# Performance work log

Measured on AMD Instinct MI355X. Metric: run time of the kernel, lower is better.

## Reference

```python
import jax, jax.numpy as jnp
import numpy as np

N_NODES = 20000
N_EDGES = 80000
D = 128       # in_dim_node == in_dim_edge == hidden dims
ITERS = 15    # mp_iterations
EPS = 1e-5    # torch LayerNorm default eps


def _mlp(h, W0, b0, W1, b1, W2, b2, gamma, beta):
    """Linear-ReLU-Linear-ReLU-Linear-LayerNorm (hidden_layers=2)."""
    h = jax.nn.relu(h @ W0 + b0)
    h = jax.nn.relu(h @ W1 + b1)
    h = h @ W2 + b2
    mu = jnp.mean(h, axis=-1, keepdims=True)
    var = jnp.var(h, axis=-1, keepdims=True)
    return gamma * (h - mu) * jax.lax.rsqrt(var + EPS) + beta


def setup_inputs() -> dict:
    key = jax.random.key(0)
    ks = iter(jax.random.split(key, 32))

    def lin(fi, fo):
        bnd = 1.0 / np.sqrt(fi)
        W = jax.random.uniform(next(ks), (ITERS, fi, fo), minval=-bnd, maxval=bnd, dtype=jnp.float32)
        b = jax.random.uniform(next(ks), (ITERS, fo), minval=-bnd, maxval=bnd, dtype=jnp.float32)
        return W, b

    x = jax.random.normal(next(ks), (N_NODES, D), dtype=jnp.float32)
    edge_attr = jax.random.normal(next(ks), (N_EDGES, D), dtype=jnp.float32)
    edge_index = jax.random.randint(next(ks), (2, N_EDGES), 0, N_NODES)

    eW0, eB0 = lin(3 * D, D)   # edge MLP input = cat(src, dest, edge) = 384
    eW1, eB1 = lin(D, D)
    eW2, eB2 = lin(D, D)
    nW0, nB0 = lin(2 * D, D)   # node MLP input = cat(x, agg) = 256
    nW1, nB1 = lin(D, D)
    nW2, nB2 = lin(D, D)
    ones = jnp.ones((ITERS, D), jnp.float32)
    zeros = jnp.zeros((ITERS, D), jnp.float32)

    return dict(x=x, edge_attr=edge_attr,
                eW0=eW0, eB0=eB0, eW1=eW1, eB1=eB1, eW2=eW2, eB2=eB2, eG=ones, eBeta=zeros,
                nW0=nW0, nB0=nB0, nW1=nW1, nB1=nB1, nW2=nW2, nB2=nB2, nG=ones, nBeta=zeros,
                edge_index=edge_index)


def reference(x, edge_attr, eW0, eB0, eW1, eB1, eW2, eB2, eG, eBeta,
              nW0, nB0, nW1, nB1, nW2, nB2, nG, nBeta, edge_index):
    row, col = edge_index[0], edge_index[1]
    n = x.shape[0]
    params = (eW0, eB0, eW1, eB1, eW2, eB2, eG, eBeta,
              nW0, nB0, nW1, nB1, nW2, nB2, nG, nBeta)

    def step(carry, p):
        xc, ec = carry
        (ew0, eb0, ew1, eb1, ew2, eb2, eg, ebt,
         nw0, nb0, nw1, nb1, nw2, nb2, ng, nbt) = p
        # EdgeProcessor: gather + MLP, then FullResidualConnection (add previous)
        e_in = jnp.concatenate([xc[row], xc[col], ec], axis=-1)        # [E, 3D]
        ec = _mlp(e_in, ew0, eb0, ew1, eb1, ew2, eb2, eg, ebt) + ec
        # NodeProcessor: scatter_sum over destination nodes + MLP + residual
        agg = jax.ops.segment_sum(ec, col, num_segments=n)             # [N, D]
        n_in = jnp.concatenate([xc, agg], axis=-1)                     # [N, 2D]
        xc = _mlp(n_in, nw0, nb0, nw1, nb1, nw2, nb2, ng, nbt) + xc
        return (xc, ec), None

    (x, edge_attr), _ = jax.lax.scan(step, (x, edge_attr), params)
    return x, edge_attr
```

## Files before the change

### kernel.cpp

```cpp
#include <hip/hip_runtime.h>
#include <hip/hip_bf16.h>

typedef __hip_bfloat16 bf16;
typedef __attribute__((ext_vector_type(8))) short short8;
typedef __attribute__((ext_vector_type(4))) float f32x4;

#define NN 20000
#define NE 80000
#define DD 128
#define NITER 15
#define HSTRIDE 136

__device__ inline void gload16(const void* g, void* l) {
  __builtin_amdgcn_global_load_lds(
      (const __attribute__((address_space(1))) void*)g,
      (__attribute__((address_space(3))) void*)l, 16, 0, 0);
}

__device__ inline void waitVm(int n) {
  switch (n) {
    case 0: asm volatile("s_waitcnt vmcnt(0)" ::: "memory"); break;
    case 1: asm volatile("s_waitcnt vmcnt(1)" ::: "memory"); break;
    case 2: asm volatile("s_waitcnt vmcnt(2)" ::: "memory"); break;
    case 3: asm volatile("s_waitcnt vmcnt(3)" ::: "memory"); break;
    case 4: asm volatile("s_waitcnt vmcnt(4)" ::: "memory"); break;
    case 5: asm volatile("s_waitcnt vmcnt(5)" ::: "memory"); break;
    default: asm volatile("s_waitcnt vmcnt(6)" ::: "memory"); break;
  }
}

__device__ inline float bfbits2f(unsigned int hi16) {
  union { unsigned int u; float f; } c; c.u = hi16; return c.f;
}

__device__ inline float readin(const void* p, size_t i, int fl) {
  return fl ? (float)((const bf16*)p)[i] : ((const float*)p)[i];
}

__global__ void detzero_kernel(const unsigned short* __restrict__ x,
                               int* __restrict__ counts, int* __restrict__ flag) {
  const int bid = blockIdx.x, t = threadIdx.x;
  if (bid < 79) {
    int i = bid * 256 + t;
    if (i < NN) counts[i] = 0;
    return;
  }
  __shared__ int cs[256], ct[256];
  int sane = 0, tot = 0;
  for (int i = 2 * t; i < 16384; i += 512) {
    unsigned short v = x[i];
    int e = (v >> 7) & 0xFF;
    tot++;
    if (v == 0 || (e >= 80 && e <= 170)) sane++;
  }
  cs[t] = sane; ct[t] = tot;
  __syncthreads();
  for (int o = 128; o > 0; o >>= 1) {
    if (t < o) { cs[t] += cs[t + o]; ct[t] += ct[t + o]; }
    __syncthreads();
  }
  if (t == 0) *flag = (cs[0] * 10 > ct[0] * 7) ? 1 : 0;
}

#define CX  (NN * DD)
#define CE  (NE * DD)
#define CW0 (NITER * 384 * DD)
#define CW1 (NITER * 128 * DD)
#define CNW0 (NITER * 256 * DD)
#define CB  (NITER * DD)
#define BX0 CX
#define BX1 (BX0 + CE)
#define BX2 (BX1 + 10 * CB)

struct CvtP {
  const void *x, *e;
  bf16 *xb, *eb;
  const void* bs[10];
  float* bd[10];
  const int* flag;
};

__global__ void convert_all(CvtP P) {
  const int fl = *P.flag;
  const int gstride = gridDim.x * 256;
  for (int i = blockIdx.x * 256 + threadIdx.x; i < BX2; i += gstride) {
    if (i < BX0) {
      P.xb[i] = (bf16)readin(P.x, i, fl);
    } else if (i < BX1) {
      P.eb[i - BX0] = (bf16)readin(P.e, i - BX0, fl);
    } else {
      int j = i - BX1;
      int b = j / CB, r = j - b * CB;
      P.bd[b][r] = readin(P.bs[b], r, fl);
    }
  }
}

struct WtP {
  const void* w[6];
  bf16* wt[6];
  const int* flag;
};

__global__ void wtrans_kernel(WtP P) {
  __shared__ float tile[32][33];
  const int fl = *P.flag;
  const int bid = blockIdx.x;
  int w, rem;
  if      (bid < 720)  { w = 0; rem = bid; }
  else if (bid < 960)  { w = 1; rem = bid - 720; }
  else if (bid < 1200) { w = 2; rem = bid - 960; }
  else if (bid < 1680) { w = 3; rem = bid - 1200; }
  else if (bid < 1920) { w = 4; rem = bid - 1680; }
  else                 { w = 5; rem = bid - 1920; }
  const int K = (w == 0) ? 384 : (w == 3) ? 256 : 128;
  const int nkt    = K >> 5;
  const int per_it = nkt << 2;
  const int it = rem / per_it;
  const int r2 = rem - it * per_it;
  const int k0 = (r2 >> 2) << 5;
  const int n0 = (r2 & 3) << 5;

  const int tx = threadIdx.x & 31, ty = threadIdx.x >> 5;
  const size_t base = (size_t)it * K * DD;

#pragma unroll
  for (int p = 0; p < 4; p++) {
    const int k = k0 + ty + 8 * p;
    tile[ty + 8 * p][tx] = readin(P.w[w], base + (size_t)k * DD + n0 + tx, fl);
  }
  __syncthreads();
#pragma unroll
  for (int p = 0; p < 4; p++) {
    const int n = n0 + ty + 8 * p;
    const int k = k0 + tx;
    const int q = (k >> 3) & 3;
    const int kp = (k & ~24) | (((q ^ ((n >> 1) & 3)) & 3) << 3);
    P.wt[w][base + (size_t)n * K + kp] = (bf16)tile[tx][ty + 8 * p];
  }
}

template<int K0, int AMODE, int NW, int MI>
__global__ __launch_bounds__(NW * 64, MI == 2 ? 3 : 4) void fused_mlp(
    const bf16* S0b,
    const bf16* S1b,
    const int*  __restrict__ eidx,
    const bf16* __restrict__ W0t, const bf16* __restrict__ W1t,
    const bf16* __restrict__ W2t,
    const float* __restrict__ b0, const float* __restrict__ b1,
    const float* __restrict__ b2,
    const float* __restrict__ gamma, const float* __restrict__ beta,
    bf16* st, int M)
{
  constexpr int NS1  = K0 / 32;
  constexpr int RPW  = 16 * MI;
  constexpr int ROWS = NW * RPW;
  constexpr int DN   = 2;
  __shared__ __align__(16) bf16 Bls[2][128 * 32];
  __shared__ __align__(16) bf16 Hls[ROWS * HSTRIDE];

  const int tid  = threadIdx.x;
  const int lane = tid & 63;
  const int wv   = tid >> 6;
  const int l15  = lane & 15, quad = lane >> 4;
  const int m0   = blockIdx.x * ROWS;
  const int scol = tid >> 2;
  const int sk8  = (tid & 3) * 8;

  int rowm[MI], ir[MI], ic[MI];
#pragma unroll
  for (int g = 0; g < MI; g++) {
    rowm[g] = min(m0 + wv * RPW + g * 16 + l15, M - 1);
    ir[g] = 0; ic[g] = 0;
    if (AMODE == 1) { ir[g] = eidx[rowm[g]]; ic[g] = eidx[NE + rowm[g]]; }
  }

  auto dmaW = [&](const bf16* W, int K, int kk, int buf) {
    gload16(W + (size_t)scol * K + kk + sk8,        &Bls[buf][scol * 32 + sk8]);
    gload16(W + (size_t)(scol + 64) * K + kk + sk8, &Bls[buf][(scol + 64) * 32 + sk8]);
  };
  auto gatherA = [&](int g, int kk, short8* a) {
    const int ks = (kk & 127) + quad * 8;
    const bf16* base;
    if (AMODE == 1) {
      const int seg = kk >> 7;
      base = (seg == 0) ? S0b + (size_t)ir[g] * DD
           : (seg == 1) ? S0b + (size_t)ic[g] * DD
                        : S1b + (size_t)rowm[g] * DD;
    } else {
      base = (kk >> 7) ? S1b + (size_t)rowm[g] * DD
                       : S0b + (size_t)rowm[g] * DD;
    }
    *a = *(const short8*)(base + ks);
  };

  auto readB = [&](int buf, short8* bfr) {
#pragma unroll
    for (int ni = 0; ni < 8; ni++) {
      const int r = ni * 16 + l15;
      bfr[ni] = *(const short8*)&Bls[buf][r * 32 + ((quad ^ ((r >> 1) & 3)) & 3) * 8];
    }
  };

  f32x4 acc[MI][8];
  auto zacc = [&]() {
#pragma unroll
    for (int g = 0; g < MI; g++)
#pragma unroll
      for (int j = 0; j < 8; j++) acc[g][j] = (f32x4){0.f, 0.f, 0.f, 0.f};
  };
  auto slabMfmaA = [&](short8* a, int buf) {
    short8 bfr[8];
    readB(buf, bfr);
#pragma unroll
    for (int g = 0; g < MI; g++)
#pragma unroll
      for (int ni = 0; ni < 8; ni++)
        acc[g][ni] = __builtin_amdgcn_mfma_f32_16x16x32_bf16(a[g], bfr[ni], acc[g][ni], 0, 0, 0);
  };
  auto slabMfmaH = [&](int kk, int buf) {
    short8 bfr[8];
    readB(buf, bfr);
#pragma unroll
    for (int g = 0; g < MI; g++) {
      short8 a = *(const short8*)&Hls[(wv * RPW + g * 16 + l15) * HSTRIDE + kk + quad * 8];
#pragma unroll
      for (int ni = 0; ni < 8; ni++)
        acc[g][ni] = __builtin_amdgcn_mfma_f32_16x16x32_bf16(a, bfr[ni], acc[g][ni], 0, 0, 0);
    }
  };
  auto writeH = [&](const float* bias) {
    float bv[8];
#pragma unroll
    for (int ni = 0; ni < 8; ni++) bv[ni] = bias[ni * 16 + l15];
#pragma unroll
    for (int g = 0; g < MI; g++)
#pragma unroll
      for (int r = 0; r < 4; r++) {
        const int row = wv * RPW + g * 16 + quad * 4 + r;
#pragma unroll
        for (int ni = 0; ni < 8; ni++)
          Hls[row * HSTRIDE + ni * 16 + l15] = (bf16)fmaxf(acc[g][ni][r] + bv[ni], 0.f);
      }
  };

  zacc();
  short8 aCur[MI], aNxt[MI];
  dmaW(W0t, K0, 0, 0);
#pragma unroll
  for (int g = 0; g < MI; g++) gatherA(g, 0, &aCur[g]);
#pragma unroll
  for (int s = 0; s < NS1; s++) {
    int cnt;
    if (s + 1 < NS1) {
      dmaW(W0t, K0, (s + 1) * 32, (s + 1) & 1);
#pragma unroll
      for (int g = 0; g < MI; g++) gatherA(g, (s + 1) * 32, &aNxt[g]);
      cnt = MI + DN + MI;
    } else {
      dmaW(W1t, 128, 0, NS1 & 1);
      cnt = MI + DN;
    }
    waitVm(cnt);
    __builtin_amdgcn_s_barrier();
    __builtin_amdgcn_sched_barrier(0);
    slabMfmaA(aCur, s & 1);
    __builtin_amdgcn_sched_barrier(0);
    __builtin_amdgcn_s_barrier();
#pragma unroll
    for (int g = 0; g < MI; g++) aCur[g] = aNxt[g];
  }
  writeH(b0);

  zacc();
#pragma unroll
  for (int s = 0; s < 4; s++) {
    if (s < 3) dmaW(W1t, 128, (s + 1) * 32, (NS1 + s + 1) & 1);
    else       dmaW(W2t, 128, 0,            (NS1 + 4) & 1);
    waitVm(DN);
    __builtin_amdgcn_s_barrier();
    __builtin_amdgcn_sched_barrier(0);
    slabMfmaH(s * 32, (NS1 + s) & 1);
    __builtin_amdgcn_sched_barrier(0);
    __builtin_amdgcn_s_barrier();
  }
  writeH(b1);

  zacc();
#pragma unroll
  for (int s = 0; s < 4; s++) {
    int cnt = 0;
    if (s < 3) { dmaW(W2t, 128, (s + 1) * 32, (NS1 + 4 + s + 1) & 1); cnt = DN; }
    waitVm(cnt);
    __builtin_amdgcn_s_barrier();
    __builtin_amdgcn_sched_barrier(0);
    slabMfmaH(s * 32, (NS1 + 4 + s) & 1);
    if (s < 3) {
      __builtin_amdgcn_sched_barrier(0);
      __builtin_amdgcn_s_barrier();
    }
  }

  float bv[8], gv[8], btv[8];
#pragma unroll
  for (int ni = 0; ni < 8; ni++) {
    const int col = ni * 16 + l15;
    bv[ni] = b2[col]; gv[ni] = gamma[col]; btv[ni] = beta[col];
  }
#pragma unroll
  for (int g = 0; g < MI; g++) {
#pragma unroll
    for (int r = 0; r < 4; r++) {
      float a = 0.f, bq = 0.f;
#pragma unroll
      for (int ni = 0; ni < 8; ni++) {
        const float v = acc[g][ni][r] + bv[ni];
        a += v; bq += v * v;
      }
#pragma unroll
      for (int off = 1; off < 16; off <<= 1) {
        a  += __shfl_xor(a, off);
        bq += __shfl_xor(bq, off);
      }
      const float mu = a * (1.0f / 128.0f);
      const float var = fmaxf(bq * (1.0f / 128.0f) - mu * mu, 0.0f);
      const float rs = rsqrtf(var + 1e-5f);
      const int m = m0 + wv * RPW + g * 16 + quad * 4 + r;
      if (m < M) {
#pragma unroll
        for (int ni = 0; ni < 8; ni++) {
          const int col = ni * 16 + l15;
          const float v = acc[g][ni][r] + bv[ni];
          const float lnv = (v - mu) * rs * gv[ni] + btv[ni];
          const size_t idx = (size_t)m * DD + col;
          st[idx] = (bf16)(lnv + (float)st[idx]);
        }
      }
    }
  }
}

__global__ void hist_kernel(const int* __restrict__ eidx, int* __restrict__ counts) {
  int e = blockIdx.x * 256 + threadIdx.x;
  if (e < NE) atomicAdd(&counts[eidx[NE + e]], 1);
}

__global__ void scan_kernel(const int* __restrict__ counts, int* __restrict__ offs,
                            int* __restrict__ cursor) {
  __shared__ int sums[1024];
  const int t = threadIdx.x;
  const int base = t * 20;
  int local[20];
  int s = 0;
  for (int i = 0; i < 20; i++) {
    int idx = base + i;
    int c = (idx < NN) ? counts[idx] : 0;
    local[i] = s; s += c;
  }
  sums[t] = s;
  __syncthreads();
  for (int off = 1; off < 1024; off <<= 1) {
    int v = 0;
    if (t >= off) v = sums[t - off];
    __syncthreads();
    if (t >= off) sums[t] += v;
    __syncthreads();
  }
  int excl = (t == 0) ? 0 : sums[t - 1];
  for (int i = 0; i < 20; i++) {
    int idx = base + i;
    if (idx < NN) { offs[idx] = excl + local[i]; cursor[idx] = 0; }
  }
  if (t == 1023) offs[NN] = sums[1023];
}

__global__ void fill_kernel(const int* __restrict__ eidx, const int* __restrict__ offs,
                            int* __restrict__ cursor, int* __restrict__ sorted) {
  int e = blockIdx.x * 256 + threadIdx.x;
  if (e < NE) {
    int n = eidx[NE + e];
    int p = atomicAdd(&cursor[n], 1);
    sorted[offs[n] + p] = e;
  }
}

__global__ void aggregate_kernel(const bf16* __restrict__ eb, const int* __restrict__ offs,
                                 const int* __restrict__ sorted, bf16* __restrict__ aggb) {
  const int node = blockIdx.x * 4 + (threadIdx.x >> 6);
  const int lane = threadIdx.x & 63;
  if (node >= NN) return;
  const int s = offs[node], t = offs[node + 1];
  float a0 = 0.f, a1 = 0.f;
  for (int i = s; i < t; i++) {
    const int e = sorted[i];
    unsigned int v = *(const unsigned int*)(eb + (size_t)e * DD + 2 * lane);
    a0 += bfbits2f(v << 16);
    a1 += bfbits2f(v & 0xFFFF0000u);
  }
  bf16 o0 = (bf16)a0, o1 = (bf16)a1;
  unsigned int pack = (unsigned int)(*(unsigned short*)&o0)
                    | ((unsigned int)(*(unsigned short*)&o1) << 16);
  *(unsigned int*)(aggb + (size_t)node * DD + 2 * lane) = pack;
}

__global__ void outwb_kernel(const bf16* __restrict__ xb, const bf16* __restrict__ eb,
                             void* __restrict__ out, const int* __restrict__ flag) {
  int i = blockIdx.x * 256 + threadIdx.x;
  const int nx = NN * DD, total = (NN + NE) * DD;
  if (i < total) {
    bf16 v = (i < nx) ? xb[i] : eb[i - nx];
    if (*flag) ((bf16*)out)[i] = v;
    else       ((float*)out)[i] = (float)v;
  }
}

extern "C" void kernel_launch(void* const* d_in, const int* in_sizes, int n_in,
                              void* d_out, int out_size, void* d_ws, size_t ws_size,
                              hipStream_t stream) {
  const int* eidx = (const int*)d_in[18];

  char* ws = (char*)d_ws;
  size_t off = 0;
  auto alloc = [&](size_t bytes) -> char* {
    char* p = ws + off;
    off = (off + bytes + 255) & ~(size_t)255;
    return p;
  };

  bf16* xb   = (bf16*)alloc((size_t)NN * DD * 2);
  bf16* eb   = (bf16*)alloc((size_t)NE * DD * 2);
  bf16* aggb = (bf16*)alloc((size_t)NN * DD * 2);
  bf16* eW0t = (bf16*)alloc((size_t)CW0 * 2);
  bf16* eW1t = (bf16*)alloc((size_t)CW1 * 2);
  bf16* eW2t = (bf16*)alloc((size_t)CW1 * 2);
  bf16* nW0t = (bf16*)alloc((size_t)CNW0 * 2);
  bf16* nW1t = (bf16*)alloc((size_t)CW1 * 2);
  bf16* nW2t = (bf16*)alloc((size_t)CW1 * 2);
  float* bf_[10];
  for (int i = 0; i < 10; i++) bf_[i] = (float*)alloc(CB * 4);
  int* counts = (int*)alloc((size_t)NN * 4);
  int* cursor = (int*)alloc((size_t)NN * 4);
  int* offs   = (int*)alloc((size_t)(NN + 1) * 4);
  int* sorted = (int*)alloc((size_t)NE * 4);
  int* flag   = (int*)alloc(4);

  detzero_kernel<<<80, 256, 0, stream>>>((const unsigned short*)d_in[0], counts, flag);

  CvtP C;
  C.x = d_in[0]; C.e = d_in[1];
  C.xb = xb; C.eb = eb;
  const int bsrc_idx[10] = {3, 5, 7, 8, 9, 11, 13, 15, 16, 17};
  for (int i = 0; i < 10; i++) { C.bs[i] = d_in[bsrc_idx[i]]; C.bd[i] = bf_[i]; }
  C.flag = flag;
  convert_all<<<2048, 256, 0, stream>>>(C);

  WtP W;
  W.w[0] = d_in[2];  W.w[1] = d_in[4];  W.w[2] = d_in[6];
  W.w[3] = d_in[10]; W.w[4] = d_in[12]; W.w[5] = d_in[14];
  W.wt[0] = eW0t; W.wt[1] = eW1t; W.wt[2] = eW2t;
  W.wt[3] = nW0t; W.wt[4] = nW1t; W.wt[5] = nW2t;
  W.flag = flag;
  wtrans_kernel<<<2160, 256, 0, stream>>>(W);

  hist_kernel<<<(NE + 255) / 256, 256, 0, stream>>>(eidx, counts);
  scan_kernel<<<1, 1024, 0, stream>>>(counts, offs, cursor);
  fill_kernel<<<(NE + 255) / 256, 256, 0, stream>>>(eidx, offs, cursor, sorted);

  const int egrid = NE / 128;
  const int ngrid = (NN + 63) / 64;

  for (int t = 0; t < NITER; t++) {
    fused_mlp<384, 1, 4, 2><<<egrid, 256, 0, stream>>>(
        xb, eb, eidx,
        eW0t + (size_t)t * 384 * DD, eW1t + (size_t)t * 128 * DD,
        eW2t + (size_t)t * 128 * DD,
        bf_[0] + t * DD, bf_[1] + t * DD, bf_[2] + t * DD,
        bf_[3] + t * DD, bf_[4] + t * DD, eb, NE);
    aggregate_kernel<<<(NN + 3) / 4, 256, 0, stream>>>(eb, offs, sorted, aggb);
    fused_mlp<256, 2, 4, 1><<<ngrid, 256, 0, stream>>>(
        xb, aggb, nullptr,
        nW0t + (size_t)t * 256 * DD, nW1t + (size_t)t * 128 * DD,
        nW2t + (size_t)t * 128 * DD,
        bf_[5] + t * DD, bf_[6] + t * DD, bf_[7] + t * DD,
        bf_[8] + t * DD, bf_[9] + t * DD, xb, NN);
  }

  outwb_kernel<<<((NN + NE) * DD + 255) / 256, 256, 0, stream>>>(xb, eb, d_out, flag);
}
```

Before: 1.065 ms.

## Fuse edge scatter-sum into edge MLP epilogue via fp32 atomics

Drops the CSR sort (hist/scan/fill) and the separate aggregate kernel. The edge MLP epilogue now atomically adds each updated edge row into an fp32 node buffer. The node MLP reads that buffer directly, converting to bf16, and re-zeroes its own rows after the first layer, ready for the next iteration. This removes one kernel launch per iteration and a re-read of the edge features, at the cost of many global fp32 atomics, a doubled-size aggregate buffer, and a summation order that is no longer deterministic.

```diff
diff --git a/kernel.cpp b/kernel.cpp
--- a/kernel.cpp
+++ b/kernel.cpp
@@ -29,22 +29,13 @@
   }
 }
 
-__device__ inline float bfbits2f(unsigned int hi16) {
-  union { unsigned int u; float f; } c; c.u = hi16; return c.f;
-}
-
 __device__ inline float readin(const void* p, size_t i, int fl) {
   return fl ? (float)((const bf16*)p)[i] : ((const float*)p)[i];
 }
 
-__global__ void detzero_kernel(const unsigned short* __restrict__ x,
-                               int* __restrict__ counts, int* __restrict__ flag) {
-  const int bid = blockIdx.x, t = threadIdx.x;
-  if (bid < 79) {
-    int i = bid * 256 + t;
-    if (i < NN) counts[i] = 0;
-    return;
-  }
+__global__ void detect_kernel(const unsigned short* __restrict__ x,
+                              int* __restrict__ flag) {
+  const int t = threadIdx.x;
   __shared__ int cs[256], ct[256];
   int sane = 0, tot = 0;
   for (int i = 2 * t; i < 16384; i += 512) {
@@ -71,27 +62,31 @@
 #define BX0 CX
 #define BX1 (BX0 + CE)
 #define BX2 (BX1 + 10 * CB)
+#define BX3 (BX2 + CX)
 
 struct CvtP {
   const void *x, *e;
   bf16 *xb, *eb;
   const void* bs[10];
   float* bd[10];
+  float* aggz;
   const int* flag;
 };
 
 __global__ void convert_all(CvtP P) {
   const int fl = *P.flag;
   const int gstride = gridDim.x * 256;
-  for (int i = blockIdx.x * 256 + threadIdx.x; i < BX2; i += gstride) {
+  for (int i = blockIdx.x * 256 + threadIdx.x; i < BX3; i += gstride) {
     if (i < BX0) {
       P.xb[i] = (bf16)readin(P.x, i, fl);
     } else if (i < BX1) {
       P.eb[i - BX0] = (bf16)readin(P.e, i - BX0, fl);
-    } else {
+    } else if (i < BX2) {
       int j = i - BX1;
       int b = j / CB, r = j - b * CB;
       P.bd[b][r] = readin(P.bs[b], r, fl);
+    } else {
+      P.aggz[i - BX2] = 0.f;
     }
   }
 }
@@ -150,7 +145,7 @@
     const float* __restrict__ b0, const float* __restrict__ b1,
     const float* __restrict__ b2,
     const float* __restrict__ gamma, const float* __restrict__ beta,
-    bf16* st, int M)
+    bf16* st, int M, float* aggf)
 {
   constexpr int NS1  = K0 / 32;
   constexpr int RPW  = 16 * MI;
@@ -181,17 +176,28 @@
   };
   auto gatherA = [&](int g, int kk, short8* a) {
     const int ks = (kk & 127) + quad * 8;
-    const bf16* base;
     if (AMODE == 1) {
       const int seg = kk >> 7;
-      base = (seg == 0) ? S0b + (size_t)ir[g] * DD
-           : (seg == 1) ? S0b + (size_t)ic[g] * DD
-                        : S1b + (size_t)rowm[g] * DD;
+      const bf16* base = (seg == 0) ? S0b + (size_t)ir[g] * DD
+                       : (seg == 1) ? S0b + (size_t)ic[g] * DD
+                                    : S1b + (size_t)rowm[g] * DD;
+      *a = *(const short8*)(base + ks);
     } else {
-      base = (kk >> 7) ? S1b + (size_t)rowm[g] * DD
-                       : S0b + (size_t)rowm[g] * DD;
-    }
-    *a = *(const short8*)(base + ks);
+      if (kk >> 7) {
+        const float* fb = aggf + (size_t)rowm[g] * DD + ks;
+        f32x4 f0 = *(const f32x4*)fb;
+        f32x4 f1 = *(const f32x4*)(fb + 4);
+        short8 r;
+#pragma unroll
+        for (int j = 0; j < 4; j++) {
+          bf16 h0 = (bf16)f0[j]; r[j]     = *(const short*)&h0;
+          bf16 h1 = (bf16)f1[j]; r[j + 4] = *(const short*)&h1;
+        }
+        *a = r;
+      } else {
+        *a = *(const short8*)(S0b + (size_t)rowm[g] * DD + ks);
+      }
+    }
   };
 
   auto readB = [&](int buf, short8* bfr) {
@@ -256,7 +262,8 @@
       dmaW(W0t, K0, (s + 1) * 32, (s + 1) & 1);
 #pragma unroll
       for (int g = 0; g < MI; g++) gatherA(g, (s + 1) * 32, &aNxt[g]);
-      cnt = MI + DN + MI;
+      const int gops = (AMODE == 2 && (((s + 1) * 32) >> 7)) ? 2 : MI;
+      cnt = MI + DN + gops;
     } else {
       dmaW(W1t, 128, 0, NS1 & 1);
       cnt = MI + DN;
@@ -271,6 +278,16 @@
     for (int g = 0; g < MI; g++) aCur[g] = aNxt[g];
   }
   writeH(b0);
+
+  if (AMODE == 2) {
+    const int rmax = min(M - m0, ROWS);
+    if (rmax > 0) {
+      f32x4* dst = (f32x4*)(aggf + (size_t)m0 * DD);
+      const int tot = rmax * (DD / 4);
+      for (int idx = tid; idx < tot; idx += NW * 64)
+        dst[idx] = (f32x4){0.f, 0.f, 0.f, 0.f};
+    }
+  }
 
   zacc();
 #pragma unroll
@@ -327,80 +344,22 @@
       const float rs = rsqrtf(var + 1e-5f);
       const int m = m0 + wv * RPW + g * 16 + quad * 4 + r;
       if (m < M) {
+        int dn = 0;
+        if (AMODE == 1) dn = eidx[NE + m];
 #pragma unroll
         for (int ni = 0; ni < 8; ni++) {
           const int col = ni * 16 + l15;
           const float v = acc[g][ni][r] + bv[ni];
           const float lnv = (v - mu) * rs * gv[ni] + btv[ni];
           const size_t idx = (size_t)m * DD + col;
-          st[idx] = (bf16)(lnv + (float)st[idx]);
+          bf16 stv = (bf16)(lnv + (float)st[idx]);
+          st[idx] = stv;
+          if (AMODE == 1)
+            atomicAdd(&aggf[(size_t)dn * DD + col], (float)stv);
         }
       }
     }
   }
-}
-
-__global__ void hist_kernel(const int* __restrict__ eidx, int* __restrict__ counts) {
-  int e = blockIdx.x * 256 + threadIdx.x;
-  if (e < NE) atomicAdd(&counts[eidx[NE + e]], 1);
-}
-
-__global__ void scan_kernel(const int* __restrict__ counts, int* __restrict__ offs,
-                            int* __restrict__ cursor) {
-  __shared__ int sums[1024];
-  const int t = threadIdx.x;
-  const int base = t * 20;
-  int local[20];
-  int s = 0;
-  for (int i = 0; i < 20; i++) {
-    int idx = base + i;
-    int c = (idx < NN) ? counts[idx] : 0;
-    local[i] = s; s += c;
-  }
-  sums[t] = s;
-  __syncthreads();
-  for (int off = 1; off < 1024; off <<= 1) {
-    int v = 0;
-    if (t >= off) v = sums[t - off];
-    __syncthreads();
-    if (t >= off) sums[t] += v;
-    __syncthreads();
-  }
-  int excl = (t == 0) ? 0 : sums[t - 1];
-  for (int i = 0; i < 20; i++) {
-    int idx = base + i;
-    if (idx < NN) { offs[idx] = excl + local[i]; cursor[idx] = 0; }
-  }
-  if (t == 1023) offs[NN] = sums[1023];
-}
-
-__global__ void fill_kernel(const int* __restrict__ eidx, const int* __restrict__ offs,
-                            int* __restrict__ cursor, int* __restrict__ sorted) {
-  int e = blockIdx.x * 256 + threadIdx.x;
-  if (e < NE) {
-    int n = eidx[NE + e];
-    int p = atomicAdd(&cursor[n], 1);
-    sorted[offs[n] + p] = e;
-  }
-}
-
-__global__ void aggregate_kernel(const bf16* __restrict__ eb, const int* __restrict__ offs,
-                                 const int* __restrict__ sorted, bf16* __restrict__ aggb) {
-  const int node = blockIdx.x * 4 + (threadIdx.x >> 6);
-  const int lane = threadIdx.x & 63;
-  if (node >= NN) return;
-  const int s = offs[node], t = offs[node + 1];
-  float a0 = 0.f, a1 = 0.f;
-  for (int i = s; i < t; i++) {
-    const int e = sorted[i];
-    unsigned int v = *(const unsigned int*)(eb + (size_t)e * DD + 2 * lane);
-    a0 += bfbits2f(v << 16);
-    a1 += bfbits2f(v & 0xFFFF0000u);
-  }
-  bf16 o0 = (bf16)a0, o1 = (bf16)a1;
-  unsigned int pack = (unsigned int)(*(unsigned short*)&o0)
-                    | ((unsigned int)(*(unsigned short*)&o1) << 16);
-  *(unsigned int*)(aggb + (size_t)node * DD + 2 * lane) = pack;
 }
 
 __global__ void outwb_kernel(const bf16* __restrict__ xb, const bf16* __restrict__ eb,
@@ -427,30 +386,27 @@
     return p;
   };
 
-  bf16* xb   = (bf16*)alloc((size_t)NN * DD * 2);
-  bf16* eb   = (bf16*)alloc((size_t)NE * DD * 2);
-  bf16* aggb = (bf16*)alloc((size_t)NN * DD * 2);
-  bf16* eW0t = (bf16*)alloc((size_t)CW0 * 2);
-  bf16* eW1t = (bf16*)alloc((size_t)CW1 * 2);
-  bf16* eW2t = (bf16*)alloc((size_t)CW1 * 2);
-  bf16* nW0t = (bf16*)alloc((size_t)CNW0 * 2);
-  bf16* nW1t = (bf16*)alloc((size_t)CW1 * 2);
-  bf16* nW2t = (bf16*)alloc((size_t)CW1 * 2);
+  bf16*  xb   = (bf16*)alloc((size_t)NN * DD * 2);
+  bf16*  eb   = (bf16*)alloc((size_t)NE * DD * 2);
+  float* aggf = (float*)alloc((size_t)NN * DD * 4);
+  bf16*  eW0t = (bf16*)alloc((size_t)CW0 * 2);
+  bf16*  eW1t = (bf16*)alloc((size_t)CW1 * 2);
+  bf16*  eW2t = (bf16*)alloc((size_t)CW1 * 2);
+  bf16*  nW0t = (bf16*)alloc((size_t)CNW0 * 2);
+  bf16*  nW1t = (bf16*)alloc((size_t)CW1 * 2);
+  bf16*  nW2t = (bf16*)alloc((size_t)CW1 * 2);
   float* bf_[10];
   for (int i = 0; i < 10; i++) bf_[i] = (float*)alloc(CB * 4);
-  int* counts = (int*)alloc((size_t)NN * 4);
-  int* cursor = (int*)alloc((size_t)NN * 4);
-  int* offs   = (int*)alloc((size_t)(NN + 1) * 4);
-  int* sorted = (int*)alloc((size_t)NE * 4);
-  int* flag   = (int*)alloc(4);
-
-  detzero_kernel<<<80, 256, 0, stream>>>((const unsigned short*)d_in[0], counts, flag);
+  int*   flag = (int*)alloc(4);
+
+  detect_kernel<<<1, 256, 0, stream>>>((const unsigned short*)d_in[0], flag);
 
   CvtP C;
   C.x = d_in[0]; C.e = d_in[1];
   C.xb = xb; C.eb = eb;
   const int bsrc_idx[10] = {3, 5, 7, 8, 9, 11, 13, 15, 16, 17};
   for (int i = 0; i < 10; i++) { C.bs[i] = d_in[bsrc_idx[i]]; C.bd[i] = bf_[i]; }
+  C.aggz = aggf;
   C.flag = flag;
   convert_all<<<2048, 256, 0, stream>>>(C);
 
@@ -462,10 +418,6 @@
   W.flag = flag;
   wtrans_kernel<<<2160, 256, 0, stream>>>(W);
 
-  hist_kernel<<<(NE + 255) / 256, 256, 0, stream>>>(eidx, counts);
-  scan_kernel<<<1, 1024, 0, stream>>>(counts, offs, cursor);
-  fill_kernel<<<(NE + 255) / 256, 256, 0, stream>>>(eidx, offs, cursor, sorted);
-
   const int egrid = NE / 128;
   const int ngrid = (NN + 63) / 64;
 
@@ -475,14 +427,13 @@
         eW0t + (size_t)t * 384 * DD, eW1t + (size_t)t * 128 * DD,
         eW2t + (size_t)t * 128 * DD,
         bf_[0] + t * DD, bf_[1] + t * DD, bf_[2] + t * DD,
-        bf_[3] + t * DD, bf_[4] + t * DD, eb, NE);
-    aggregate_kernel<<<(NN + 3) / 4, 256, 0, stream>>>(eb, offs, sorted, aggb);
+        bf_[3] + t * DD, bf_[4] + t * DD, eb, NE, aggf);
     fused_mlp<256, 2, 4, 1><<<ngrid, 256, 0, stream>>>(
-        xb, aggb, nullptr,
+        xb, nullptr, nullptr,
         nW0t + (size_t)t * 256 * DD, nW1t + (size_t)t * 128 * DD,
         nW2t + (size_t)t * 128 * DD,
         bf_[5] + t * DD, bf_[6] + t * DD, bf_[7] + t * DD,
-        bf_[8] + t * DD, bf_[9] + t * DD, xb, NN);
+        bf_[8] + t * DD, bf_[9] + t * DD, xb, NN, aggf);
   }
 
   outwb_kernel<<<((NN + NE) * DD + 255) / 256, 256, 0, stream>>>(xb, eb, d_out, flag);
```

Result: slower. 1.290 ms (+21.1%).
